# Optimization experiments

Hardware: AMD Instinct MI355X
Metric: run time of the kernel (lower is better)

## Reference

```python
import jax, jax.numpy as jnp
import numpy as np

N = 100000      # nodes
E = 1600000     # edges (avg degree 16)
IN = 128        # in_channels
H = 128         # hidden_channels
OUT = 64        # out_channels
NHID = 3        # num_layers (hidden->hidden SAGE convs)


def _lin(k, fan_out, fan_in):
    s = 1.0 / np.sqrt(fan_in)
    return jax.random.uniform(k, (fan_out, fan_in), jnp.float32, -s, s)


def setup_inputs() -> dict:
    key = jax.random.key(0)
    ks = jax.random.split(key, 12)
    x = jax.random.normal(ks[0], (N, IN), dtype=jnp.float32)
    edge_index = jax.random.randint(ks[1], (2, E), 0, N, dtype=jnp.int32)
    # inProj Linear(IN -> H)
    Wp = _lin(ks[2], H, IN)
    bp = jnp.zeros((H,), jnp.float32)
    # 3 hidden SAGEConv(H -> H): lin_l (with bias) on aggregated neighbors, lin_r (no bias) on root
    Wl_h = jnp.stack([_lin(jax.random.fold_in(ks[3], i), H, H) for i in range(NHID)])
    bl_h = jnp.zeros((NHID, H), jnp.float32)
    Wr_h = jnp.stack([_lin(jax.random.fold_in(ks[4], i), H, H) for i in range(NHID)])
    # output SAGEConv(H -> OUT)
    Wl_o = _lin(ks[5], OUT, H)
    bl_o = jnp.zeros((OUT,), jnp.float32)
    Wr_o = _lin(ks[6], OUT, H)
    return {"x": x, "edge_index": edge_index, "Wp": Wp, "bp": bp,
            "Wl_h": Wl_h, "bl_h": bl_h, "Wr_h": Wr_h,
            "Wl_o": Wl_o, "bl_o": bl_o, "Wr_o": Wr_o}


def reference(x, edge_index, Wp, bp, Wl_h, bl_h, Wr_h, Wl_o, bl_o, Wr_o):
    src, dst = edge_index[0], edge_index[1]
    ones = jnp.ones((E,), x.dtype)
    deg = jax.ops.segment_sum(ones, dst, num_segments=N)           # [N]
    inv_deg = (1.0 / jnp.maximum(deg, 1.0))[:, None]               # [N,1]

    def sage(h, Wl, bl, Wr):
        # mean aggregation of source features onto destinations (irregular gather+scatter)
        s = jax.ops.segment_sum(h[src], dst, num_segments=N)       # [N,d]
        mean = s * inv_deg
        return mean @ Wl.T + bl + h @ Wr.T

    h = x @ Wp.T + bp
    inp = h
    h = jax.nn.relu(h)
    for i in range(NHID):
        h = sage(h, Wl_h[i], bl_h[i], Wr_h[i])
        h = jax.nn.relu(h)                                          # dropout is identity in eval
        h = h + 0.2 * inp
    h = sage(h, Wl_o, bl_o, Wr_o)
    return jax.nn.log_softmax(h, axis=-1)
```

## Files before the change

### kernel.cpp

```cpp
#include <hip/hip_runtime.h>
#include <math.h>

#define N_NODES 100000
#define N_EDGES 1600000
#define NBUK 391
#define PCHUNK 8192
#define NPBLK 196

typedef unsigned short u16;
typedef unsigned char u8;
typedef __bf16 bf16x8 __attribute__((ext_vector_type(8)));
typedef float f32x4 __attribute__((ext_vector_type(4)));
typedef float f32x2 __attribute__((ext_vector_type(2)));

#define OFF_RP      0u
#define OFF_INVDEG  400016u
#define OFF_BHIST   800016u
#define OFF_BBASE   801600u
#define OFF_GCUR    803200u
#define OFF_PAIRS   804800u
#define OFF_COL     13604800u
#define OFF_PACK    20004800u
#define OFF_INP     20266944u
#define OFF_H       45866944u
#define OFF_H8A     71466944u
#define OFF_H8B     84266944u
#define OFF_GL      97066944u
#define OFF_GR      109866944u
#define WS_NEEDED   122666944u

#define PK_WP   0
#define PK_WL   16384
#define PK_WR   65536
#define PK_WLO  114688
#define PK_WRO  122880

__device__ __forceinline__ float bfl(unsigned u) {
  union { unsigned i; float f; } v; v.i = u << 16; return v.f;
}
__device__ __forceinline__ float bfh(unsigned u) {
  union { unsigned i; float f; } v; v.i = u & 0xFFFF0000u; return v.f;
}
__device__ __forceinline__ u16 f2b(float f) {
  union { float f; unsigned i; } v; v.f = f;
  unsigned r = (v.i + 0x7FFFu + ((v.i >> 16) & 1u)) >> 16;
  return (u16)r;
}

__global__ __launch_bounds__(256) void pack_weights_k(
    const float* __restrict__ Wp, const float* __restrict__ Wl,
    const float* __restrict__ Wr, const float* __restrict__ Wlo,
    const float* __restrict__ Wro, u16* __restrict__ P) {
  int t = blockIdx.x * 256 + threadIdx.x;
  if (t >= 16384) return;
  const float* W; u16* dst; int j; int NT;
  if (t < 2048)        { W = Wp;                    dst = P + PK_WP;                j = t;                 NT = 8; }
  else if (t < 8192)   { int m = (t - 2048) >> 11;  j = (t - 2048) & 2047;
                         W = Wl + (m << 14);        dst = P + PK_WL + (m << 14);    NT = 8; }
  else if (t < 14336)  { int m = (t - 8192) >> 11;  j = (t - 8192) & 2047;
                         W = Wr + (m << 14);        dst = P + PK_WR + (m << 14);    NT = 8; }
  else if (t < 15360)  { j = t - 14336;             W = Wlo;  dst = P + PK_WLO;     NT = 4; }
  else                 { j = t - 15360;             W = Wro;  dst = P + PK_WRO;     NT = 4; }
  int lane = j & 63;
  int nt, kt;
  if (NT == 8) { nt = (j >> 6) & 7; kt = j >> 9; }
  else         { nt = (j >> 6) & 3; kt = j >> 8; }
  int n  = nt * 16 + (lane & 15);
  int k0 = kt * 32 + ((lane >> 4) << 3);
  const float* s = W + n * 128 + k0;
  ushort4 lo = make_ushort4(f2b(s[0]), f2b(s[1]), f2b(s[2]), f2b(s[3]));
  ushort4 hi = make_ushort4(f2b(s[4]), f2b(s[5]), f2b(s[6]), f2b(s[7]));
  *(ushort4*)(dst + j * 8)     = lo;
  *(ushort4*)(dst + j * 8 + 4) = hi;
}

__global__ __launch_bounds__(256) void bhist_k(const int* __restrict__ dst,
                                               int* __restrict__ bhist) {
  __shared__ int lc[NBUK];
  int t = threadIdx.x;
  for (int i = t; i < NBUK; i += 256) lc[i] = 0;
  __syncthreads();
  int base = blockIdx.x * 4096;
#pragma unroll
  for (int r = 0; r < 16; r++) {
    int i = base + r * 256 + t;
    if (i < N_EDGES) atomicAdd(&lc[dst[i] >> 8], 1);
  }
  __syncthreads();
  for (int i = t; i < NBUK; i += 256)
    if (lc[i]) atomicAdd(&bhist[i], lc[i]);
}

__global__ __launch_bounds__(512) void bscan_k(const int* __restrict__ bhist,
                                               int* __restrict__ bbase,
                                               int* __restrict__ gcur,
                                               int* __restrict__ rp) {
  __shared__ int s[512];
  int t = threadIdx.x;
  int v = (t < NBUK) ? bhist[t] : 0;
  s[t] = v;
  __syncthreads();
  for (int off = 1; off < 512; off <<= 1) {
    int u = (t >= off) ? s[t - off] : 0;
    __syncthreads();
    s[t] += u;
    __syncthreads();
  }
  if (t < NBUK) { int e = s[t] - v; bbase[t] = e; gcur[t] = e; }
  if (t == NBUK - 1) { bbase[NBUK] = s[t]; rp[N_NODES] = s[t]; }
}

__global__ __launch_bounds__(256) void part_k(const int* __restrict__ src,
                                              const int* __restrict__ dst,
                                              int* __restrict__ gcur,
                                              uint2* __restrict__ pairs) {
  __shared__ int lcnt[NBUK + 1];
  __shared__ int lofs[512];
  __shared__ int cur[NBUK];
  __shared__ int gslot[NBUK];
  __shared__ uint2 stag[PCHUNK];
  int t = threadIdx.x;
  for (int i = t; i < NBUK + 1; i += 256) lcnt[i] = 0;
  __syncthreads();
  int base = blockIdx.x * PCHUNK;
#pragma unroll
  for (int r = 0; r < PCHUNK / 256; r++) {
    int i = base + r * 256 + t;
    if (i < N_EDGES) atomicAdd(&lcnt[dst[i] >> 8], 1);
  }
  __syncthreads();
  {
    int e1 = t + 256;
    lofs[t]  = (t  <= NBUK) ? lcnt[t]  : 0;
    lofs[e1] = (e1 <= NBUK) ? lcnt[e1] : 0;
    __syncthreads();
    for (int off = 1; off < 512; off <<= 1) {
      int a0 = (t  >= off) ? lofs[t  - off] : 0;
      int a1 = (e1 >= off) ? lofs[e1 - off] : 0;
      __syncthreads();
      lofs[t] += a0; lofs[e1] += a1;
      __syncthreads();
    }
    int o0 = lofs[t]  - ((t  <= NBUK) ? lcnt[t]  : 0);
    int o1 = lofs[e1] - ((e1 <= NBUK) ? lcnt[e1] : 0);
    __syncthreads();
    lofs[t] = o0; lofs[e1] = o1;
    __syncthreads();
  }
  for (int i = t; i < NBUK; i += 256) cur[i] = lofs[i];
  __syncthreads();
#pragma unroll
  for (int r = 0; r < PCHUNK / 256; r++) {
    int i = base + r * 256 + t;
    if (i < N_EDGES) {
      int d = dst[i];
      int slot = atomicAdd(&cur[d >> 8], 1);
      stag[slot] = make_uint2((unsigned)src[i], (unsigned)d);
    }
  }
  __syncthreads();
  for (int i = t; i < NBUK; i += 256)
    if (lcnt[i]) gslot[i] = atomicAdd(&gcur[i], lcnt[i]);
  __syncthreads();
  int total = lofs[NBUK];
  for (int p = t; p < total; p += 256) {
    uint2 pr = stag[p];
    int b = (int)(pr.y >> 8);
    pairs[gslot[b] + (p - lofs[b])] = pr;
  }
}

__global__ __launch_bounds__(256) void csr_k(const uint2* __restrict__ pairs,
                                             const int* __restrict__ bbase,
                                             int* __restrict__ rp,
                                             float* __restrict__ invdeg,
                                             int* __restrict__ col) {
  __shared__ int cnt[256];
  __shared__ int scn[256];
  __shared__ int cur[256];
  int b = blockIdx.x, t = threadIdx.x;
  int lo = bbase[b], hi = bbase[b + 1];
  cnt[t] = 0;
  __syncthreads();
  for (int p = lo + t; p < hi; p += 256)
    atomicAdd(&cnt[pairs[p].y & 255], 1);
  __syncthreads();
  int c = cnt[t];
  scn[t] = c;
  __syncthreads();
  for (int off = 1; off < 256; off <<= 1) {
    int v = (t >= off) ? scn[t - off] : 0;
    __syncthreads();
    scn[t] += v;
    __syncthreads();
  }
  int excl = scn[t] - c;
  int node = (b << 8) + t;
  if (node < N_NODES) {
    rp[node] = lo + excl;
    invdeg[node] = 1.0f / (float)(c > 1 ? c : 1);
  }
  cur[t] = lo + excl;
  __syncthreads();
  for (int p = lo + t; p < hi; p += 256) {
    uint2 pr = pairs[p];
    int slot = atomicAdd(&cur[pr.y & 255], 1);
    col[slot] = (int)pr.x;
  }
}

__global__ __launch_bounds__(256) void inproj_mfma_k(
    const float* __restrict__ X, const u16* __restrict__ P,
    const float* __restrict__ bias,
    u16* __restrict__ inp, u16* __restrict__ hout, u8* __restrict__ h8out, int M) {
  __shared__ float zb[64 * 132];
  int tid = threadIdx.x;
  int w = tid >> 6, lane = tid & 63;
  int quad = lane >> 4, l15 = lane & 15;
  int m0 = blockIdx.x * 64;
  int rowa = m0 + w * 16 + l15; if (rowa > M - 1) rowa = M - 1;
  f32x4 acc[8] = {};
#pragma unroll
  for (int kt = 0; kt < 4; kt++) {
    const float* xr = X + (long)rowa * 128 + kt * 32 + quad * 8;
    float4 p0 = *(const float4*)xr;
    float4 p1 = *(const float4*)(xr + 4);
    union { ushort4 u4[2]; bf16x8 v; } fa;
    fa.u4[0] = make_ushort4(f2b(p0.x), f2b(p0.y), f2b(p0.z), f2b(p0.w));
    fa.u4[1] = make_ushort4(f2b(p1.x), f2b(p1.y), f2b(p1.z), f2b(p1.w));
    const u16* pb = P + ((kt * 8) * 64 + lane) * 8;
#pragma unroll
    for (int nt = 0; nt < 8; nt++) {
      bf16x8 bf = *(const bf16x8*)(pb + nt * 512);
      acc[nt] = __builtin_amdgcn_mfma_f32_16x16x32_bf16(fa.v, bf, acc[nt], 0, 0, 0);
    }
  }
#pragma unroll
  for (int nt = 0; nt < 8; nt++) {
    int c = nt * 16 + l15;
    float b = bias[c];
#pragma unroll
    for (int r = 0; r < 4; r++)
      zb[(w * 16 + quad * 4 + r) * 132 + c] = acc[nt][r] + b;
  }
  __syncthreads();
  int r = lane >> 2, seg = lane & 3;
  long grow = m0 + w * 16 + r;
  if (grow < M) {
    const float* zrow = &zb[(w * 16 + r) * 132 + seg * 32];
    u16* ip = inp + grow * 128 + seg * 32;
    u16* hp = hout + grow * 128 + seg * 32;
    u8*  qp = h8out + grow * 128 + seg * 32;
#pragma unroll
    for (int b = 0; b < 4; b++) {
      float zv[8];
      *(float4*)&zv[0] = *(const float4*)(zrow + b * 8);
      *(float4*)&zv[4] = *(const float4*)(zrow + b * 8 + 4);
      float rv[8];
#pragma unroll
      for (int jj = 0; jj < 8; jj++) rv[jj] = fmaxf(zv[jj], 0.f);
      *(ushort4*)(ip + b * 8)     = make_ushort4(f2b(zv[0]), f2b(zv[1]), f2b(zv[2]), f2b(zv[3]));
      *(ushort4*)(ip + b * 8 + 4) = make_ushort4(f2b(zv[4]), f2b(zv[5]), f2b(zv[6]), f2b(zv[7]));
      *(ushort4*)(hp + b * 8)     = make_ushort4(f2b(rv[0]), f2b(rv[1]), f2b(rv[2]), f2b(rv[3]));
      *(ushort4*)(hp + b * 8 + 4) = make_ushort4(f2b(rv[4]), f2b(rv[5]), f2b(rv[6]), f2b(rv[7]));
      unsigned q0 = 0, q1 = 0;
      q0 = __builtin_amdgcn_cvt_pk_fp8_f32(rv[0], rv[1], q0, false);
      q0 = __builtin_amdgcn_cvt_pk_fp8_f32(rv[2], rv[3], q0, true);
      q1 = __builtin_amdgcn_cvt_pk_fp8_f32(rv[4], rv[5], q1, false);
      q1 = __builtin_amdgcn_cvt_pk_fp8_f32(rv[6], rv[7], q1, true);
      *(uint2*)(qp + b * 8) = make_uint2(q0, q1);
    }
  }
}

__global__ __launch_bounds__(256) void sage_fused_k(
    const u8* __restrict__ h8, const int* __restrict__ rp,
    const int* __restrict__ col, const float* __restrict__ invdeg,
    u16* __restrict__ h, const u16* __restrict__ PL, const u16* __restrict__ PR,
    const float* __restrict__ bias, const u16* __restrict__ inp,
    u8* __restrict__ h8out, int M) {
  __shared__ float zb[8448];
  u16* meanT = (u16*)zb;
  int tid = threadIdx.x;
  int m0 = blockIdx.x * 64;
  {
    int hw = tid >> 5, lane = tid & 31;
    const u8* hp = h8 + lane * 4;
#pragma unroll 1
    for (int it = 0; it < 8; it++) {
      int node = m0 + it * 8 + hw;
      if (node < M) {
        int beg = rp[node], end = rp[node + 1];
        float a0 = 0.f, a1 = 0.f, a2 = 0.f, a3 = 0.f;
        int j = beg;
        for (; j + 3 < end; j += 4) {
          int s0 = col[j], s1 = col[j + 1], s2 = col[j + 2], s3 = col[j + 3];
          unsigned v0 = *(const unsigned*)(hp + ((long)s0 << 7));
          unsigned v1 = *(const unsigned*)(hp + ((long)s1 << 7));
          unsigned v2 = *(const unsigned*)(hp + ((long)s2 << 7));
          unsigned v3 = *(const unsigned*)(hp + ((long)s3 << 7));
          f32x2 p0 = __builtin_amdgcn_cvt_pk_f32_fp8(v0, false);
          f32x2 p1 = __builtin_amdgcn_cvt_pk_f32_fp8(v0, true);
          f32x2 p2 = __builtin_amdgcn_cvt_pk_f32_fp8(v1, false);
          f32x2 p3 = __builtin_amdgcn_cvt_pk_f32_fp8(v1, true);
          f32x2 p4 = __builtin_amdgcn_cvt_pk_f32_fp8(v2, false);
          f32x2 p5 = __builtin_amdgcn_cvt_pk_f32_fp8(v2, true);
          f32x2 p6 = __builtin_amdgcn_cvt_pk_f32_fp8(v3, false);
          f32x2 p7 = __builtin_amdgcn_cvt_pk_f32_fp8(v3, true);
          a0 += (p0[0] + p2[0]) + (p4[0] + p6[0]);
          a1 += (p0[1] + p2[1]) + (p4[1] + p6[1]);
          a2 += (p1[0] + p3[0]) + (p5[0] + p7[0]);
          a3 += (p1[1] + p3[1]) + (p5[1] + p7[1]);
        }
        for (; j < end; j++) {
          unsigned v0 = *(const unsigned*)(hp + ((long)col[j] << 7));
          f32x2 p0 = __builtin_amdgcn_cvt_pk_f32_fp8(v0, false);
          f32x2 p1 = __builtin_amdgcn_cvt_pk_f32_fp8(v0, true);
          a0 += p0[0]; a1 += p0[1]; a2 += p1[0]; a3 += p1[1];
        }
        float wd = invdeg[node];
        *(ushort4*)&meanT[(it * 8 + hw) * 136 + lane * 4] =
            make_ushort4(f2b(a0 * wd), f2b(a1 * wd), f2b(a2 * wd), f2b(a3 * wd));
      }
    }
  }
  __syncthreads();
  int w = tid >> 6, lane = tid & 63;
  int quad = lane >> 4, l15 = lane & 15;
  int rowa = m0 + w * 16 + l15; if (rowa > M - 1) rowa = M - 1;
  f32x4 acc[8] = {};
#pragma unroll
  for (int kt = 0; kt < 4; kt++) {
    bf16x8 am = *(const bf16x8*)&meanT[(w * 16 + l15) * 136 + kt * 32 + quad * 8];
    bf16x8 ar = *(const bf16x8*)(h + (long)rowa * 128 + kt * 32 + quad * 8);
    const u16* pl = PL + ((kt * 8) * 64 + lane) * 8;
    const u16* pr = PR + ((kt * 8) * 64 + lane) * 8;
#pragma unroll
    for (int nt = 0; nt < 8; nt++) {
      bf16x8 b0 = *(const bf16x8*)(pl + nt * 512);
      bf16x8 b1 = *(const bf16x8*)(pr + nt * 512);
      acc[nt] = __builtin_amdgcn_mfma_f32_16x16x32_bf16(am, b0, acc[nt], 0, 0, 0);
      acc[nt] = __builtin_amdgcn_mfma_f32_16x16x32_bf16(ar, b1, acc[nt], 0, 0, 0);
    }
  }
  __syncthreads();
#pragma unroll
  for (int nt = 0; nt < 8; nt++) {
    int c = nt * 16 + l15;
    float b = bias[c];
#pragma unroll
    for (int r = 0; r < 4; r++)
      zb[(w * 16 + quad * 4 + r) * 132 + c] = fmaxf(acc[nt][r] + b, 0.f);
  }
  __syncthreads();
  int r = lane >> 2, seg = lane & 3;
  long grow = m0 + w * 16 + r;
  if (grow < M) {
    const float* zrow = &zb[(w * 16 + r) * 132 + seg * 32];
    const u16* ip = inp + grow * 128 + seg * 32;
    u16* op = h + grow * 128 + seg * 32;
#pragma unroll
    for (int b = 0; b < 4; b++) {
      float zv[8];
      *(float4*)&zv[0] = *(const float4*)(zrow + b * 8);
      *(float4*)&zv[4] = *(const float4*)(zrow + b * 8 + 4);
      uint2 iv0 = *(const uint2*)(ip + b * 8);
      uint2 iv1 = *(const uint2*)(ip + b * 8 + 4);
      float fv[8];
      fv[0] = zv[0] + 0.2f * bfl(iv0.x); fv[1] = zv[1] + 0.2f * bfh(iv0.x);
      fv[2] = zv[2] + 0.2f * bfl(iv0.y); fv[3] = zv[3] + 0.2f * bfh(iv0.y);
      fv[4] = zv[4] + 0.2f * bfl(iv1.x); fv[5] = zv[5] + 0.2f * bfh(iv1.x);
      fv[6] = zv[6] + 0.2f * bfl(iv1.y); fv[7] = zv[7] + 0.2f * bfh(iv1.y);
      *(ushort4*)(op + b * 8)     = make_ushort4(f2b(fv[0]), f2b(fv[1]), f2b(fv[2]), f2b(fv[3]));
      *(ushort4*)(op + b * 8 + 4) = make_ushort4(f2b(fv[4]), f2b(fv[5]), f2b(fv[6]), f2b(fv[7]));
      if (h8out) {
        unsigned q0 = 0, q1 = 0;
        q0 = __builtin_amdgcn_cvt_pk_fp8_f32(fv[0], fv[1], q0, false);
        q0 = __builtin_amdgcn_cvt_pk_fp8_f32(fv[2], fv[3], q0, true);
        q1 = __builtin_amdgcn_cvt_pk_fp8_f32(fv[4], fv[5], q1, false);
        q1 = __builtin_amdgcn_cvt_pk_fp8_f32(fv[6], fv[7], q1, true);
        *(uint2*)(h8out + grow * 128 + seg * 32 + b * 8) = make_uint2(q0, q1);
      }
    }
  }
}

__global__ __launch_bounds__(256) void out_proj_k(
    const u16* __restrict__ A, const u16* __restrict__ PLO,
    const u16* __restrict__ PRO, u16* __restrict__ gl, u16* __restrict__ gr, int M) {
  __shared__ float zb[64 * 132];
  int tid = threadIdx.x;
  int w = tid >> 6, lane = tid & 63;
  int quad = lane >> 4, l15 = lane & 15;
  int m0 = blockIdx.x * 64;
  int rowa = m0 + w * 16 + l15; if (rowa > M - 1) rowa = M - 1;
  f32x4 acc[8] = {};
#pragma unroll
  for (int kt = 0; kt < 4; kt++) {
    bf16x8 af = *(const bf16x8*)(A + (long)rowa * 128 + kt * 32 + quad * 8);
#pragma unroll
    for (int nt = 0; nt < 4; nt++) {
      bf16x8 b0 = *(const bf16x8*)(PLO + ((kt * 4 + nt) * 64 + lane) * 8);
      bf16x8 b1 = *(const bf16x8*)(PRO + ((kt * 4 + nt) * 64 + lane) * 8);
      acc[nt]     = __builtin_amdgcn_mfma_f32_16x16x32_bf16(af, b0, acc[nt], 0, 0, 0);
      acc[4 + nt] = __builtin_amdgcn_mfma_f32_16x16x32_bf16(af, b1, acc[4 + nt], 0, 0, 0);
    }
  }
#pragma unroll
  for (int nt = 0; nt < 4; nt++) {
    int c = nt * 16 + l15;
#pragma unroll
    for (int r = 0; r < 4; r++) {
      zb[(w * 16 + quad * 4 + r) * 132 + c]      = acc[nt][r];
      zb[(w * 16 + quad * 4 + r) * 132 + 64 + c] = acc[4 + nt][r];
    }
  }
  __syncthreads();
  int r = lane >> 2, seg = lane & 3;
  long grow = m0 + w * 16 + r;
  if (grow < M) {
    const float* zrow = &zb[(w * 16 + r) * 132 + seg * 32];
    u16* dp = (seg < 2) ? (gl + grow * 64 + seg * 32) : (gr + grow * 64 + (seg - 2) * 32);
#pragma unroll
    for (int b = 0; b < 4; b++) {
      float zv[8];
      *(float4*)&zv[0] = *(const float4*)(zrow + b * 8);
      *(float4*)&zv[4] = *(const float4*)(zrow + b * 8 + 4);
      *(ushort4*)(dp + b * 8)     = make_ushort4(f2b(zv[0]), f2b(zv[1]), f2b(zv[2]), f2b(zv[3]));
      *(ushort4*)(dp + b * 8 + 4) = make_ushort4(f2b(zv[4]), f2b(zv[5]), f2b(zv[6]), f2b(zv[7]));
    }
  }
}

__global__ __launch_bounds__(256) void out_final_k(
    const u16* __restrict__ gl, const u16* __restrict__ gr,
    const float* __restrict__ blo, const int* __restrict__ rp,
    const int* __restrict__ col, const float* __restrict__ invdeg,
    float* __restrict__ outp) {
  int node = blockIdx.x * 8 + (threadIdx.x >> 5);
  int lane = threadIdx.x & 31;
  if (node >= N_NODES) return;
  int beg = rp[node], end = rp[node + 1];
  const u16* glp = gl + lane * 2;
  float a0 = 0.f, a1 = 0.f;
  int j = beg;
  for (; j + 3 < end; j += 4) {
    int s0 = col[j], s1 = col[j + 1], s2 = col[j + 2], s3 = col[j + 3];
    unsigned v0 = *(const unsigned*)(glp + ((long)s0 << 6));
    unsigned v1 = *(const unsigned*)(glp + ((long)s1 << 6));
    unsigned v2 = *(const unsigned*)(glp + ((long)s2 << 6));
    unsigned v3 = *(const unsigned*)(glp + ((long)s3 << 6));
    a0 += (bfl(v0) + bfl(v1)) + (bfl(v2) + bfl(v3));
    a1 += (bfh(v0) + bfh(v1)) + (bfh(v2) + bfh(v3));
  }
  for (; j < end; j++) {
    unsigned v0 = *(const unsigned*)(glp + ((long)col[j] << 6));
    a0 += bfl(v0); a1 += bfh(v0);
  }
  float wd = invdeg[node];
  unsigned g = *(const unsigned*)(gr + (long)node * 64 + lane * 2);
  float z0 = a0 * wd + bfl(g) + blo[lane * 2];
  float z1 = a1 * wd + bfh(g) + blo[lane * 2 + 1];
  float mx = fmaxf(z0, z1);
#pragma unroll
  for (int off = 16; off >= 1; off >>= 1) mx = fmaxf(mx, __shfl_xor(mx, off, 32));
  float s = __expf(z0 - mx) + __expf(z1 - mx);
#pragma unroll
  for (int off = 16; off >= 1; off >>= 1) s += __shfl_xor(s, off, 32);
  float ro = mx + __logf(s);
  float2 o = make_float2(z0 - ro, z1 - ro);
  *(float2*)(outp + (long)node * 64 + lane * 2) = o;
}

extern "C" void kernel_launch(void* const* d_in, const int* in_sizes, int n_in,
                              void* d_out, int out_size, void* d_ws, size_t ws_size,
                              hipStream_t stream) {
  if (ws_size < (size_t)WS_NEEDED) return;
  const float* x   = (const float*)d_in[0];
  const int*   ei  = (const int*)d_in[1];
  const float* Wp  = (const float*)d_in[2];
  const float* bp  = (const float*)d_in[3];
  const float* Wl  = (const float*)d_in[4];
  const float* bl  = (const float*)d_in[5];
  const float* Wr  = (const float*)d_in[6];
  const float* Wlo = (const float*)d_in[7];
  const float* blo = (const float*)d_in[8];
  const float* Wro = (const float*)d_in[9];
  float* out = (float*)d_out;
  char* ws = (char*)d_ws;
  int*   rp     = (int*)(ws + OFF_RP);
  float* invdeg = (float*)(ws + OFF_INVDEG);
  int*   bhist  = (int*)(ws + OFF_BHIST);
  int*   bbase  = (int*)(ws + OFF_BBASE);
  int*   gcur   = (int*)(ws + OFF_GCUR);
  uint2* pairs  = (uint2*)(ws + OFF_PAIRS);
  int*   col    = (int*)(ws + OFF_COL);
  u16*   pack   = (u16*)(ws + OFF_PACK);
  u16*   inp    = (u16*)(ws + OFF_INP);
  u16*   h      = (u16*)(ws + OFF_H);
  u8*    h8a    = (u8*)(ws + OFF_H8A);
  u8*    h8b    = (u8*)(ws + OFF_H8B);
  u16*   gl     = (u16*)(ws + OFF_GL);
  u16*   gr     = (u16*)(ws + OFF_GR);
  const int* srcv = ei;
  const int* dstv = ei + N_EDGES;

  hipMemsetAsync(ws + OFF_BHIST, 0, (NBUK + 1) * 4, stream);
  pack_weights_k<<<64, 256, 0, stream>>>(Wp, Wl, Wr, Wlo, Wro, pack);
  bhist_k<<<391, 256, 0, stream>>>(dstv, bhist);
  bscan_k<<<1, 512, 0, stream>>>(bhist, bbase, gcur, rp);
  part_k<<<NPBLK, 256, 0, stream>>>(srcv, dstv, gcur, pairs);
  csr_k<<<NBUK, 256, 0, stream>>>(pairs, bbase, rp, invdeg, col);

  int gblk = (N_NODES + 63) / 64;
  int fblk = (N_NODES + 7) / 8;

  inproj_mfma_k<<<gblk, 256, 0, stream>>>(x, pack + PK_WP, bp, inp, h, h8a, N_NODES);

  sage_fused_k<<<gblk, 256, 0, stream>>>(h8a, rp, col, invdeg, h,
                                         pack + PK_WL, pack + PK_WR, bl, inp, h8b, N_NODES);
  sage_fused_k<<<gblk, 256, 0, stream>>>(h8b, rp, col, invdeg, h,
                                         pack + PK_WL + 16384, pack + PK_WR + 16384,
                                         bl + 128, inp, h8a, N_NODES);
  sage_fused_k<<<gblk, 256, 0, stream>>>(h8a, rp, col, invdeg, h,
                                         pack + PK_WL + 32768, pack + PK_WR + 32768,
                                         bl + 256, inp, (u8*)nullptr, N_NODES);

  out_proj_k<<<gblk, 256, 0, stream>>>(h, pack + PK_WLO, pack + PK_WRO, gl, gr, N_NODES);
  out_final_k<<<fblk, 256, 0, stream>>>(gl, gr, blo, rp, col, invdeg, out);
}
```

Baseline: 615.5 us.

## Split neighbor aggregation into its own kernel and stage the mean in global memory

```diff
diff --git a/kernel.cpp b/kernel.cpp
--- a/kernel.cpp
+++ b/kernel.cpp
@@ -27,7 +27,8 @@
 #define OFF_H8B     84266944u
 #define OFF_GL      97066944u
 #define OFF_GR      109866944u
-#define WS_NEEDED   122666944u
+#define OFF_MEAN    122666944u
+#define WS_NEEDED   148266944u
 
 #define PK_WP   0
 #define PK_WL   16384
@@ -209,6 +210,48 @@
   }
 }
 
+__global__ __launch_bounds__(256) void aggregate_fp8_k(const u8* __restrict__ h8,
+                                                       const int* __restrict__ rp,
+                                                       const int* __restrict__ col,
+                                                       const float* __restrict__ invdeg,
+                                                       u16* __restrict__ mean) {
+  int node = blockIdx.x * 8 + (threadIdx.x >> 5);
+  int lane = threadIdx.x & 31;
+  if (node >= N_NODES) return;
+  int beg = rp[node], end = rp[node + 1];
+  const u8* hp = h8 + lane * 4;
+  float a0 = 0.f, a1 = 0.f, a2 = 0.f, a3 = 0.f;
+  int j = beg;
+  for (; j + 3 < end; j += 4) {
+    int s0 = col[j], s1 = col[j + 1], s2 = col[j + 2], s3 = col[j + 3];
+    unsigned v0 = *(const unsigned*)(hp + ((long)s0 << 7));
+    unsigned v1 = *(const unsigned*)(hp + ((long)s1 << 7));
+    unsigned v2 = *(const unsigned*)(hp + ((long)s2 << 7));
+    unsigned v3 = *(const unsigned*)(hp + ((long)s3 << 7));
+    f32x2 p0 = __builtin_amdgcn_cvt_pk_f32_fp8(v0, false);
+    f32x2 p1 = __builtin_amdgcn_cvt_pk_f32_fp8(v0, true);
+    f32x2 p2 = __builtin_amdgcn_cvt_pk_f32_fp8(v1, false);
+    f32x2 p3 = __builtin_amdgcn_cvt_pk_f32_fp8(v1, true);
+    f32x2 p4 = __builtin_amdgcn_cvt_pk_f32_fp8(v2, false);
+    f32x2 p5 = __builtin_amdgcn_cvt_pk_f32_fp8(v2, true);
+    f32x2 p6 = __builtin_amdgcn_cvt_pk_f32_fp8(v3, false);
+    f32x2 p7 = __builtin_amdgcn_cvt_pk_f32_fp8(v3, true);
+    a0 += (p0[0] + p2[0]) + (p4[0] + p6[0]);
+    a1 += (p0[1] + p2[1]) + (p4[1] + p6[1]);
+    a2 += (p1[0] + p3[0]) + (p5[0] + p7[0]);
+    a3 += (p1[1] + p3[1]) + (p5[1] + p7[1]);
+  }
+  for (; j < end; j++) {
+    unsigned v0 = *(const unsigned*)(hp + ((long)col[j] << 7));
+    f32x2 p0 = __builtin_amdgcn_cvt_pk_f32_fp8(v0, false);
+    f32x2 p1 = __builtin_amdgcn_cvt_pk_f32_fp8(v0, true);
+    a0 += p0[0]; a1 += p0[1]; a2 += p1[0]; a3 += p1[1];
+  }
+  float wd = invdeg[node];
+  *(ushort4*)(mean + ((long)node << 7) + lane * 4) =
+      make_ushort4(f2b(a0 * wd), f2b(a1 * wd), f2b(a2 * wd), f2b(a3 * wd));
+}
+
 __global__ __launch_bounds__(256) void inproj_mfma_k(
     const float* __restrict__ X, const u16* __restrict__ P,
     const float* __restrict__ bias,
@@ -273,68 +316,24 @@
   }
 }
 
-__global__ __launch_bounds__(256) void sage_fused_k(
-    const u8* __restrict__ h8, const int* __restrict__ rp,
-    const int* __restrict__ col, const float* __restrict__ invdeg,
-    u16* __restrict__ h, const u16* __restrict__ PL, const u16* __restrict__ PR,
+__global__ __launch_bounds__(256) void sage_mfma8_k(
+    const u16* __restrict__ A0, const u16* __restrict__ P0,
+    const u16* __restrict__ A1, const u16* __restrict__ P1,
     const float* __restrict__ bias, const u16* __restrict__ inp,
-    u8* __restrict__ h8out, int M) {
-  __shared__ float zb[8448];
-  u16* meanT = (u16*)zb;
+    u16* __restrict__ outp, u8* __restrict__ h8out, int M) {
+  __shared__ float zb[64 * 132];
   int tid = threadIdx.x;
-  int m0 = blockIdx.x * 64;
-  {
-    int hw = tid >> 5, lane = tid & 31;
-    const u8* hp = h8 + lane * 4;
-#pragma unroll 1
-    for (int it = 0; it < 8; it++) {
-      int node = m0 + it * 8 + hw;
-      if (node < M) {
-        int beg = rp[node], end = rp[node + 1];
-        float a0 = 0.f, a1 = 0.f, a2 = 0.f, a3 = 0.f;
-        int j = beg;
-        for (; j + 3 < end; j += 4) {
-          int s0 = col[j], s1 = col[j + 1], s2 = col[j + 2], s3 = col[j + 3];
-          unsigned v0 = *(const unsigned*)(hp + ((long)s0 << 7));
-          unsigned v1 = *(const unsigned*)(hp + ((long)s1 << 7));
-          unsigned v2 = *(const unsigned*)(hp + ((long)s2 << 7));
-          unsigned v3 = *(const unsigned*)(hp + ((long)s3 << 7));
-          f32x2 p0 = __builtin_amdgcn_cvt_pk_f32_fp8(v0, false);
-          f32x2 p1 = __builtin_amdgcn_cvt_pk_f32_fp8(v0, true);
-          f32x2 p2 = __builtin_amdgcn_cvt_pk_f32_fp8(v1, false);
-          f32x2 p3 = __builtin_amdgcn_cvt_pk_f32_fp8(v1, true);
-          f32x2 p4 = __builtin_amdgcn_cvt_pk_f32_fp8(v2, false);
-          f32x2 p5 = __builtin_amdgcn_cvt_pk_f32_fp8(v2, true);
-          f32x2 p6 = __builtin_amdgcn_cvt_pk_f32_fp8(v3, false);
-          f32x2 p7 = __builtin_amdgcn_cvt_pk_f32_fp8(v3, true);
-          a0 += (p0[0] + p2[0]) + (p4[0] + p6[0]);
-          a1 += (p0[1] + p2[1]) + (p4[1] + p6[1]);
-          a2 += (p1[0] + p3[0]) + (p5[0] + p7[0]);
-          a3 += (p1[1] + p3[1]) + (p5[1] + p7[1]);
-        }
-        for (; j < end; j++) {
-          unsigned v0 = *(const unsigned*)(hp + ((long)col[j] << 7));
-          f32x2 p0 = __builtin_amdgcn_cvt_pk_f32_fp8(v0, false);
-          f32x2 p1 = __builtin_amdgcn_cvt_pk_f32_fp8(v0, true);
-          a0 += p0[0]; a1 += p0[1]; a2 += p1[0]; a3 += p1[1];
-        }
-        float wd = invdeg[node];
-        *(ushort4*)&meanT[(it * 8 + hw) * 136 + lane * 4] =
-            make_ushort4(f2b(a0 * wd), f2b(a1 * wd), f2b(a2 * wd), f2b(a3 * wd));
-      }
-    }
-  }
-  __syncthreads();
   int w = tid >> 6, lane = tid & 63;
   int quad = lane >> 4, l15 = lane & 15;
+  int m0 = blockIdx.x * 64;
   int rowa = m0 + w * 16 + l15; if (rowa > M - 1) rowa = M - 1;
   f32x4 acc[8] = {};
 #pragma unroll
   for (int kt = 0; kt < 4; kt++) {
-    bf16x8 am = *(const bf16x8*)&meanT[(w * 16 + l15) * 136 + kt * 32 + quad * 8];
-    bf16x8 ar = *(const bf16x8*)(h + (long)rowa * 128 + kt * 32 + quad * 8);
-    const u16* pl = PL + ((kt * 8) * 64 + lane) * 8;
-    const u16* pr = PR + ((kt * 8) * 64 + lane) * 8;
+    bf16x8 am = *(const bf16x8*)(A0 + (long)rowa * 128 + kt * 32 + quad * 8);
+    bf16x8 ar = *(const bf16x8*)(A1 + (long)rowa * 128 + kt * 32 + quad * 8);
+    const u16* pl = P0 + ((kt * 8) * 64 + lane) * 8;
+    const u16* pr = P1 + ((kt * 8) * 64 + lane) * 8;
 #pragma unroll
     for (int nt = 0; nt < 8; nt++) {
       bf16x8 b0 = *(const bf16x8*)(pl + nt * 512);
@@ -343,7 +342,6 @@
       acc[nt] = __builtin_amdgcn_mfma_f32_16x16x32_bf16(ar, b1, acc[nt], 0, 0, 0);
     }
   }
-  __syncthreads();
 #pragma unroll
   for (int nt = 0; nt < 8; nt++) {
     int c = nt * 16 + l15;
@@ -358,7 +356,7 @@
   if (grow < M) {
     const float* zrow = &zb[(w * 16 + r) * 132 + seg * 32];
     const u16* ip = inp + grow * 128 + seg * 32;
-    u16* op = h + grow * 128 + seg * 32;
+    u16* op = outp + grow * 128 + seg * 32;
 #pragma unroll
     for (int b = 0; b < 4; b++) {
       float zv[8];
@@ -502,6 +500,7 @@
   u8*    h8b    = (u8*)(ws + OFF_H8B);
   u16*   gl     = (u16*)(ws + OFF_GL);
   u16*   gr     = (u16*)(ws + OFF_GR);
+  u16*   mean   = (u16*)(ws + OFF_MEAN);
   const int* srcv = ei;
   const int* dstv = ei + N_EDGES;
 
@@ -517,14 +516,15 @@
 
   inproj_mfma_k<<<gblk, 256, 0, stream>>>(x, pack + PK_WP, bp, inp, h, h8a, N_NODES);
 
-  sage_fused_k<<<gblk, 256, 0, stream>>>(h8a, rp, col, invdeg, h,
-                                         pack + PK_WL, pack + PK_WR, bl, inp, h8b, N_NODES);
-  sage_fused_k<<<gblk, 256, 0, stream>>>(h8b, rp, col, invdeg, h,
-                                         pack + PK_WL + 16384, pack + PK_WR + 16384,
-                                         bl + 128, inp, h8a, N_NODES);
-  sage_fused_k<<<gblk, 256, 0, stream>>>(h8a, rp, col, invdeg, h,
-                                         pack + PK_WL + 32768, pack + PK_WR + 32768,
-                                         bl + 256, inp, (u8*)nullptr, N_NODES);
+  aggregate_fp8_k<<<fblk, 256, 0, stream>>>(h8a, rp, col, invdeg, mean);
+  sage_mfma8_k<<<gblk, 256, 0, stream>>>(mean, pack + PK_WL, h, pack + PK_WR,
+                                         bl, inp, h, h8b, N_NODES);
+  aggregate_fp8_k<<<fblk, 256, 0, stream>>>(h8b, rp, col, invdeg, mean);
+  sage_mfma8_k<<<gblk, 256, 0, stream>>>(mean, pack + PK_WL + 16384, h, pack + PK_WR + 16384,
+                                         bl + 128, inp, h, h8a, N_NODES);
+  aggregate_fp8_k<<<fblk, 256, 0, stream>>>(h8a, rp, col, invdeg, mean);
+  sage_mfma8_k<<<gblk, 256, 0, stream>>>(mean, pack + PK_WL + 32768, h, pack + PK_WR + 32768,
+                                         bl + 256, inp, h, (u8*)nullptr, N_NODES);
 
   out_proj_k<<<gblk, 256, 0, stream>>>(h, pack + PK_WLO, pack + PK_WRO, gl, gr, N_NODES);
   out_final_k<<<fblk, 256, 0, stream>>>(gl, gr, blo, rp, col, invdeg, out);
```

Result: faster. 545.4 us (-11.4%).
